# Kernel optimization log

Hardware: AMD Instinct MI355X
Metric: run time of the kernel (lower is better)

## Reference

```python
import jax, jax.numpy as jnp
import numpy as np

NB = 5  # frequency bands


def _ln(x, g, b, eps=1e-5):
    m = jnp.mean(x, axis=-1, keepdims=True)
    v = jnp.var(x, axis=-1, keepdims=True)
    return (x - m) / jnp.sqrt(v + eps) * g + b


def _graph_adj(x, adj_w, sw1, sb1, sw2, sb2, pos_factor, pos_enc):
    # x: [B, D, N] -> degree-normalized adjacency [B, N, N]
    d = x.shape[1]
    xt = jnp.swapaxes(x, 1, 2)  # [B, N, D]
    # concat-MLP first layer split: cat(xi, xj) @ W1 == xi @ W1[:d] + xj @ W1[d:]
    a = xt @ sw1[:d]
    bpart = xt @ sw1[d:]
    h = jax.nn.elu(a[:, :, None, :] + bpart[:, None, :, :] + sb1)  # [B, N, N, H]
    dyn = jax.nn.sigmoid(jnp.squeeze(h @ sw2, -1) + sb2)  # [B, N, N]
    static = jax.nn.softmax(adj_w, axis=-1)
    pos = jax.nn.softmax(pos_enc, axis=-1)
    comb = jax.nn.softmax(static + dyn + pos_factor * pos, axis=-1)
    deg = jnp.sum(comb, axis=-1)
    dis = (deg + 1e-8) ** -0.5
    return dis[:, :, None] * comb * dis[:, None, :]


def _gcn(x, adj, w, b):
    # x: [B, D, N], adj: [B, N, N] -> [B, D_out, N]
    xt = jnp.swapaxes(x, 1, 2)
    out = jnp.einsum('bij,bjd->bid', adj, xt) @ w + b
    return jnp.swapaxes(out, 1, 2)


def _mha(x, qkv_w, qkv_b, ow, ob, nh=4):
    B, S, D = x.shape
    dh = D // nh
    q, k, v = jnp.split(x @ qkv_w + qkv_b, 3, axis=-1)
    q = q.reshape(B, S, nh, dh)
    k = k.reshape(B, S, nh, dh)
    v = v.reshape(B, S, nh, dh)
    att = jax.nn.softmax(jnp.einsum('bihd,bjhd->bhij', q, k) / float(np.sqrt(dh)), axis=-1)
    o = jnp.einsum('bhij,bjhd->bihd', att, v).reshape(B, S, D)
    return o @ ow + ob


def setup_inputs():
    key = jax.random.key(0)
    B, D, N = 16, 256, 64
    ks = iter(jax.random.split(key, 40))

    def rn(shape, s=0.05):
        return jax.random.normal(next(ks), shape, dtype=jnp.float32) * s

    eyeN = jnp.eye(N, dtype=jnp.float32)
    return dict(
        feature=jax.random.normal(next(ks), (B, NB * D, 1, N), dtype=jnp.float32),
        l_adj_w=jnp.tile(eyeN[None], (NB, 1, 1)),
        l_sim_w1=rn((NB, 2 * D, D)), l_sim_b1=jnp.zeros((NB, D), jnp.float32),
        l_sim_w2=rn((NB, D, 1)), l_sim_b2=jnp.zeros((NB, 1), jnp.float32),
        l_pos_factor=jnp.full((NB,), 0.5, jnp.float32),
        l_pos_enc=jnp.tile(eyeN[None], (NB, 1, 1)),
        l_gcn_w=rn((NB, D, D)), l_gcn_b=jnp.zeros((NB, D), jnp.float32),
        g_adj_w=jnp.eye(NB, dtype=jnp.float32),
        g_sim_w1=rn((2 * D, D)), g_sim_b1=jnp.zeros((D,), jnp.float32),
        g_sim_w2=rn((D, 1)), g_sim_b2=jnp.zeros((1,), jnp.float32),
        g_pos_factor=jnp.float32(0.5),
        g_pos_enc=jnp.eye(NB, dtype=jnp.float32),
        g_gcn_w=rn((D, D)), g_gcn_b=jnp.zeros((D,), jnp.float32),
        qkv_w=rn((D, 3 * D)), qkv_b=jnp.zeros((3 * D,), jnp.float32),
        attn_ow=rn((D, D)), attn_ob=jnp.zeros((D,), jnp.float32),
        ln1_g=jnp.ones((D,), jnp.float32), ln1_b=jnp.zeros((D,), jnp.float32),
        ln2_g=jnp.ones((D,), jnp.float32), ln2_b=jnp.zeros((D,), jnp.float32),
        mlp_w1=rn((D, 4 * D)), mlp_b1=jnp.zeros((4 * D,), jnp.float32),
        mlp_w2=rn((4 * D, D)), mlp_b2=jnp.zeros((D,), jnp.float32),
        imp_w=rn((NB, N, 1)), imp_b=jnp.zeros((NB, 1), jnp.float32),
    )


def reference(feature, l_adj_w, l_sim_w1, l_sim_b1, l_sim_w2, l_sim_b2,
              l_pos_factor, l_pos_enc, l_gcn_w, l_gcn_b,
              g_adj_w, g_sim_w1, g_sim_b1, g_sim_w2, g_sim_b2,
              g_pos_factor, g_pos_enc, g_gcn_w, g_gcn_b,
              qkv_w, qkv_b, attn_ow, attn_ob,
              ln1_g, ln1_b, ln2_g, ln2_b,
              mlp_w1, mlp_b1, mlp_w2, mlp_b2,
              imp_w, imp_b):
    B = feature.shape[0]
    D = l_gcn_w.shape[-1]
    N = feature.shape[-1]
    # [B, 5*D, 1, N] -> [5, B, D, N] band-major
    x5 = jnp.moveaxis(feature.reshape(B, NB, D, N), 1, 0)
    # per-band local graphs + GCNs (vmapped over the 5 bands)
    local_adj = jax.vmap(_graph_adj)(x5, l_adj_w, l_sim_w1, l_sim_b1,
                                     l_sim_w2, l_sim_b2, l_pos_factor, l_pos_enc)
    local_out = jax.vmap(_gcn)(x5, local_adj, l_gcn_w, l_gcn_b)  # [5, B, D, N]
    scale_nodes = jnp.moveaxis(jnp.mean(local_out, axis=-1), 0, 1)  # [B, 5, D]
    # cross-band attention block (pre: MHA + residual + LN, then MLP + residual + LN)
    attn = _mha(scale_nodes, qkv_w, qkv_b, attn_ow, attn_ob)
    h1 = _ln(scale_nodes + attn, ln1_g, ln1_b)
    mlp = jax.nn.gelu(h1 @ mlp_w1 + mlp_b1, approximate=False) @ mlp_w2 + mlp_b2
    se = _ln(h1 + mlp, ln2_g, ln2_b)  # [B, 5, D]
    # global scale graph over the 5 band nodes
    xg = jnp.swapaxes(se, 1, 2)  # [B, D, 5]
    g_adj = _graph_adj(xg, g_adj_w, g_sim_w1, g_sim_b1, g_sim_w2, g_sim_b2,
                       g_pos_factor, g_pos_enc)
    g_out = jnp.swapaxes(_gcn(xg, g_adj, g_gcn_w, g_gcn_b), 1, 2)  # [B, 5, D]
    # modulate each local band feature by its global scale vector
    enh = local_out * jnp.moveaxis(g_out, 1, 0)[..., None]  # [5, B, D, N]
    # per-band importance projection over channels: [5, B, D, 1]
    out5 = jnp.einsum('kbdn,kno->kbdo', enh, imp_w) + imp_b[:, None, None, :]
    output = jnp.moveaxis(out5, 0, 1).reshape(B, NB * D, 1, 1)
    return output, g_adj, jnp.moveaxis(local_out, 0, 1)
```

## Files before the change

### kernel.cpp

```cpp
#include <hip/hip_runtime.h>
#include <hip/hip_bf16.h>

#define NBANDS 5
#define BATCH  16
#define DIM    256
#define NNODE  64
#define SEQ    5
#define NHEAD  4
#define DHEAD  64

typedef __hip_bfloat16 bf16;
typedef unsigned short ushort_t;
typedef __attribute__((ext_vector_type(8))) short short8;
typedef __attribute__((ext_vector_type(4))) float float4v;

__device__ __forceinline__ float bu2f(ushort_t u){
    bf16 h = *reinterpret_cast<bf16*>(&u);
    return __bfloat162float(h);
}
__device__ __forceinline__ ushort_t f2bu(float x){
    bf16 h = __float2bfloat16(x);
    return *reinterpret_cast<ushort_t*>(&h);
}

__global__ void k_bases(const float* __restrict__ l_adj_w, const float* __restrict__ l_pos_enc,
                        const float* __restrict__ l_pf,
                        const float* __restrict__ g_adj_w, const float* __restrict__ g_pos_enc,
                        const float* __restrict__ g_pf,
                        float* __restrict__ sbase, float* __restrict__ gbase,
                        float* __restrict__ zbuf)
{
    int blk = blockIdx.x;
    int t = threadIdx.x;
    if (blk < NBANDS*NNODE) {
        int k = blk / NNODE, i = blk % NNODE;
        float aw = l_adj_w[(k*NNODE + i)*NNODE + t];
        float pe = l_pos_enc[(k*NNODE + i)*NNODE + t];
        float m1 = aw, m2 = pe;
        for (int o=32;o>0;o>>=1){ m1 = fmaxf(m1, __shfl_xor(m1,o,64)); m2 = fmaxf(m2, __shfl_xor(m2,o,64)); }
        float e1 = __expf(aw-m1), e2 = __expf(pe-m2);
        float s1=e1, s2=e2;
        for (int o=32;o>0;o>>=1){ s1 += __shfl_xor(s1,o,64); s2 += __shfl_xor(s2,o,64); }
        float pf = l_pf[k];
        sbase[(k*NNODE+i)*NNODE + t] = e1/s1 + pf*(e2/s2);
    } else if (blk == NBANDS*NNODE) {
        if (t < NBANDS) {
            int i = t;
            float r1[NBANDS], r2[NBANDS];
            float m1=-1e30f, m2=-1e30f;
            for (int j=0;j<NBANDS;j++){
                r1[j]=g_adj_w[i*NBANDS+j]; r2[j]=g_pos_enc[i*NBANDS+j];
                m1=fmaxf(m1,r1[j]); m2=fmaxf(m2,r2[j]);
            }
            float s1=0.f,s2=0.f;
            for (int j=0;j<NBANDS;j++){ r1[j]=__expf(r1[j]-m1); r2[j]=__expf(r2[j]-m2); s1+=r1[j]; s2+=r2[j]; }
            float pf = g_pf[0];
            for (int j=0;j<NBANDS;j++) gbase[i*NBANDS+j] = r1[j]/s1 + pf*(r2[j]/s2);
        }
    } else {
        for (int i=t;i<DIM;i+=64) zbuf[i] = 0.f;
    }
}

__global__ void k_prep(const float* __restrict__ w1, const float* __restrict__ gw,
                       ushort_t* __restrict__ w1bt, ushort_t* __restrict__ gwbt)
{
    int blk = blockIdx.x;
    int inst = blk >> 4;
    int t = blk & 15;
    int r0 = (t>>2)*64, c0 = (t&3)*64;
    const float* src; ushort_t* dst;
    if (inst < 10){
        int k = inst>>1, half = inst&1;
        src = w1  + ((size_t)k*512 + half*256)*256;
        dst = w1bt+ ((size_t)k*512 + half*256)*256;
    } else {
        int k = inst-10;
        src = gw  + (size_t)k*65536;
        dst = gwbt+ (size_t)k*65536;
    }
    __shared__ ushort_t tile[64][65];
    int tid = threadIdx.x;
    int jj = tid & 63, i4 = tid >> 6;
    for (int p=0;p<16;p++){
        int i = p*4 + i4;
        tile[i][jj] = f2bu(src[(size_t)(r0+i)*256 + c0 + jj]);
    }
    __syncthreads();
    for (int p=0;p<16;p++){
        int i = p*4 + i4;
        dst[(size_t)(c0+i)*256 + r0 + jj] = tile[jj][i];
    }
}

__global__ void k_transpose_feat(const float* __restrict__ feat,
                                 ushort_t* __restrict__ xtb,
                                 ushort_t* __restrict__ xtT)
{
    int k = blockIdx.x / BATCH, b = blockIdx.x % BATCH;
    __shared__ ushort_t tile[64][65];
    const float* src = feat + ((size_t)b*NBANDS*DIM + (size_t)k*DIM)*NNODE;
    ushort_t* dst = xtb + (size_t)(k*BATCH+b)*NNODE*DIM;
    int tid = threadIdx.x;
    ushort_t* dstT = xtT + (size_t)(k*BATCH+b)*DIM*NNODE;
    for (int u=0; u<64; ++u){
        int idx = u*256 + tid;
        dstT[idx] = f2bu(src[idx]);
    }
    for (int dt=0; dt<4; ++dt){
        for (int r=0;r<16;r++){
            int dp = r*4 + (tid>>6);
            int n  = tid & 63;
            tile[dp][n] = f2bu(src[(size_t)(dt*64+dp)*NNODE + n]);
        }
        __syncthreads();
        for (int r=0;r<16;r++){
            int n  = r*4 + (tid>>6);
            int dp = tid & 63;
            dst[(size_t)n*DIM + dt*64 + dp] = tile[dp][n];
        }
        __syncthreads();
    }
}

__global__ void __launch_bounds__(256) k_ab_mfma(const ushort_t* __restrict__ xtb,
                        const ushort_t* __restrict__ w1bt, const float* __restrict__ b1,
                        ushort_t* __restrict__ aab, ushort_t* __restrict__ bbb)
{
    int blk = blockIdx.x;
    int kband = blk / (BATCH*8);
    int b = (blk/8) % BATCH;
    int nblk = blk & 7;
    int tid = threadIdx.x;
    int wave = tid>>6, lane = tid&63;
    int c16 = lane & 15, quad = lane >> 4;
    int m0 = wave*16;
    size_t rowbase = (size_t)(kband*BATCH+b)*NNODE;
    const ushort_t* Aptr = xtb + (rowbase + m0 + c16)*DIM + quad*8;
    const ushort_t* Bbase = w1bt + (size_t)kband*512*DIM;
    int ncol0 = nblk*64;
    const ushort_t* Bptr0 = Bbase + (size_t)(ncol0 +  0 + c16)*DIM + quad*8;
    const ushort_t* Bptr1 = Bbase + (size_t)(ncol0 + 16 + c16)*DIM + quad*8;
    const ushort_t* Bptr2 = Bbase + (size_t)(ncol0 + 32 + c16)*DIM + quad*8;
    const ushort_t* Bptr3 = Bbase + (size_t)(ncol0 + 48 + c16)*DIM + quad*8;
    float4v acc0 = {0.f,0.f,0.f,0.f}, acc1 = acc0, acc2 = acc0, acc3 = acc0;
    #pragma unroll
    for (int ks=0; ks<8; ++ks){
        short8 a  = *reinterpret_cast<const short8*>(Aptr  + ks*32);
        short8 b0 = *reinterpret_cast<const short8*>(Bptr0 + ks*32);
        short8 b1v= *reinterpret_cast<const short8*>(Bptr1 + ks*32);
        short8 b2 = *reinterpret_cast<const short8*>(Bptr2 + ks*32);
        short8 b3 = *reinterpret_cast<const short8*>(Bptr3 + ks*32);
        acc0 = __builtin_amdgcn_mfma_f32_16x16x32_bf16(a, b0, acc0, 0,0,0);
        acc1 = __builtin_amdgcn_mfma_f32_16x16x32_bf16(a, b1v, acc1, 0,0,0);
        acc2 = __builtin_amdgcn_mfma_f32_16x16x32_bf16(a, b2, acc2, 0,0,0);
        acc3 = __builtin_amdgcn_mfma_f32_16x16x32_bf16(a, b3, acc3, 0,0,0);
    }
    int half = nblk >> 2;
    int cbase = (nblk & 3)*64;
    ushort_t* dst = half ? bbb : aab;
    float4v accs[4] = {acc0, acc1, acc2, acc3};
    #pragma unroll
    for (int nt=0; nt<4; ++nt){
        int cg = cbase + nt*16 + c16;
        float bias = half ? 0.f : b1[kband*DIM + cg];
        #pragma unroll
        for (int r=0;r<4;r++){
            int m = m0 + quad*4 + r;
            dst[(rowbase + m)*DIM + cg] = f2bu(accs[nt][r] + bias);
        }
    }
}

__global__ void k_dyn_comb(const ushort_t* __restrict__ aab,
                           const ushort_t* __restrict__ bbb,
                           const float* __restrict__ w2, const float* __restrict__ b2arr,
                           const float* __restrict__ sbase,
                           ushort_t* __restrict__ combb)
{
    int blk = blockIdx.x;
    int k = blk / (BATCH*16);
    int b = (blk / 16) % BATCH;
    int i0 = (blk % 16) * 4;
    int kb = k*BATCH + b;
    __shared__ float arows[4][DIM];
    __shared__ float w2s[DIM];
    __shared__ float dyn_s[4][NNODE];
    int tid = threadIdx.x;
    int wave = tid >> 6, lane = tid & 63;
    for (int r=0;r<4;r++) arows[r][tid] = bu2f(aab[((size_t)kb*NNODE + i0 + r)*DIM + tid]);
    w2s[tid] = w2[k*DIM + tid];
    __syncthreads();
    const ushort_t* bpbase = bbb + (size_t)kb*NNODE*DIM;
    for (int jt=0; jt<16; ++jt){
        int j = jt*4 + wave;
        const ushort_t* bj = bpbase + (size_t)j*DIM;
        float acc[4] = {0.f,0.f,0.f,0.f};
        #pragma unroll
        for (int m=0;m<4;m++){
            int dd = lane + m*64;
            float bpv = bu2f(bj[dd]);
            float wv  = w2s[dd];
            #pragma unroll
            for (int r=0;r<4;r++){
                float v = arows[r][dd] + bpv;
                float e = (v > 0.f) ? v : (__expf(v) - 1.f);
                acc[r] += e*wv;
            }
        }
        #pragma unroll
        for (int r=0;r<4;r++){
            float s = acc[r];
            for (int o=32;o>0;o>>=1) s += __shfl_xor(s,o,64);
            if (lane==0) dyn_s[r][j] = s;
        }
    }
    __syncthreads();
    {
        float sb2 = b2arr[k];
        float t = dyn_s[wave][lane] + sb2;
        float sg = 1.f/(1.f + __expf(-t));
        float val = sbase[(k*NNODE + i0 + wave)*NNODE + lane] + sg;
        float m = val;
        for (int o=32;o>0;o>>=1) m = fmaxf(m, __shfl_xor(m,o,64));
        float e = __expf(val - m);
        float s = e;
        for (int o=32;o>0;o>>=1) s += __shfl_xor(s,o,64);
        combb[((size_t)kb*NNODE + i0 + wave)*NNODE + lane] = f2bu(e/s);
    }
}

__global__ void __launch_bounds__(256) k_y_mfma(const ushort_t* __restrict__ combb,
                       const ushort_t* __restrict__ xtT,
                       ushort_t* __restrict__ yb)
{
    int blk = blockIdx.x;
    int kband = blk / (BATCH*4);
    int b = (blk/4) % BATCH;
    int nblk = blk & 3;
    int tid = threadIdx.x;
    int wave = tid>>6, lane = tid&63;
    int c16 = lane & 15, quad = lane >> 4;
    int m0 = wave*16;
    int kb = kband*BATCH + b;
    const ushort_t* Aptr = combb + ((size_t)kb*NNODE + m0 + c16)*NNODE + quad*8;
    const ushort_t* Bbase = xtT + (size_t)kb*DIM*NNODE;
    int ncol0 = nblk*64;
    const ushort_t* Bptr0 = Bbase + (size_t)(ncol0 +  0 + c16)*NNODE + quad*8;
    const ushort_t* Bptr1 = Bbase + (size_t)(ncol0 + 16 + c16)*NNODE + quad*8;
    const ushort_t* Bptr2 = Bbase + (size_t)(ncol0 + 32 + c16)*NNODE + quad*8;
    const ushort_t* Bptr3 = Bbase + (size_t)(ncol0 + 48 + c16)*NNODE + quad*8;
    float4v acc0 = {0.f,0.f,0.f,0.f}, acc1 = acc0, acc2 = acc0, acc3 = acc0;
    #pragma unroll
    for (int ks=0; ks<2; ++ks){
        short8 a  = *reinterpret_cast<const short8*>(Aptr  + ks*32);
        short8 b0 = *reinterpret_cast<const short8*>(Bptr0 + ks*32);
        short8 b1v= *reinterpret_cast<const short8*>(Bptr1 + ks*32);
        short8 b2 = *reinterpret_cast<const short8*>(Bptr2 + ks*32);
        short8 b3 = *reinterpret_cast<const short8*>(Bptr3 + ks*32);
        acc0 = __builtin_amdgcn_mfma_f32_16x16x32_bf16(a, b0, acc0, 0,0,0);
        acc1 = __builtin_amdgcn_mfma_f32_16x16x32_bf16(a, b1v, acc1, 0,0,0);
        acc2 = __builtin_amdgcn_mfma_f32_16x16x32_bf16(a, b2, acc2, 0,0,0);
        acc3 = __builtin_amdgcn_mfma_f32_16x16x32_bf16(a, b3, acc3, 0,0,0);
    }
    size_t rowbase = (size_t)kb*NNODE;
    float4v accs[4] = {acc0, acc1, acc2, acc3};
    #pragma unroll
    for (int nt=0; nt<4; ++nt){
        int cg = ncol0 + nt*16 + c16;
        #pragma unroll
        for (int r=0;r<4;r++){
            int m = m0 + quad*4 + r;
            yb[(rowbase + m)*DIM + cg] = f2bu(accs[nt][r]);
        }
    }
}

__global__ void __launch_bounds__(256) k_gcn_mfma(const ushort_t* __restrict__ yb,
                         const ushort_t* __restrict__ gwbt, const float* __restrict__ gb,
                         float* __restrict__ out_local)
{
    int blk = blockIdx.x;
    int kband = blk / (BATCH*4);
    int b = (blk/4) % BATCH;
    int nblk = blk & 3;
    int tid = threadIdx.x;
    int wave = tid>>6, lane = tid&63;
    int c16 = lane & 15, quad = lane >> 4;
    int m0 = wave*16;
    int kb = kband*BATCH + b;
    const ushort_t* Aptr = yb + ((size_t)kb*NNODE + m0 + c16)*DIM + quad*8;
    const ushort_t* Bbase = gwbt + (size_t)kband*DIM*DIM;
    int ncol0 = nblk*64;
    const ushort_t* Bptr0 = Bbase + (size_t)(ncol0 +  0 + c16)*DIM + quad*8;
    const ushort_t* Bptr1 = Bbase + (size_t)(ncol0 + 16 + c16)*DIM + quad*8;
    const ushort_t* Bptr2 = Bbase + (size_t)(ncol0 + 32 + c16)*DIM + quad*8;
    const ushort_t* Bptr3 = Bbase + (size_t)(ncol0 + 48 + c16)*DIM + quad*8;
    float4v acc0 = {0.f,0.f,0.f,0.f}, acc1 = acc0, acc2 = acc0, acc3 = acc0;
    #pragma unroll
    for (int ks=0; ks<8; ++ks){
        short8 a  = *reinterpret_cast<const short8*>(Aptr  + ks*32);
        short8 b0 = *reinterpret_cast<const short8*>(Bptr0 + ks*32);
        short8 b1v= *reinterpret_cast<const short8*>(Bptr1 + ks*32);
        short8 b2 = *reinterpret_cast<const short8*>(Bptr2 + ks*32);
        short8 b3 = *reinterpret_cast<const short8*>(Bptr3 + ks*32);
        acc0 = __builtin_amdgcn_mfma_f32_16x16x32_bf16(a, b0, acc0, 0,0,0);
        acc1 = __builtin_amdgcn_mfma_f32_16x16x32_bf16(a, b1v, acc1, 0,0,0);
        acc2 = __builtin_amdgcn_mfma_f32_16x16x32_bf16(a, b2, acc2, 0,0,0);
        acc3 = __builtin_amdgcn_mfma_f32_16x16x32_bf16(a, b3, acc3, 0,0,0);
    }
    float4v accs[4] = {acc0, acc1, acc2, acc3};
    #pragma unroll
    for (int nt=0; nt<4; ++nt){
        int cg = ncol0 + nt*16 + c16;
        float bias = gb[kband*DIM + cg];
        float4 v = make_float4(accs[nt][0]+bias, accs[nt][1]+bias, accs[nt][2]+bias, accs[nt][3]+bias);
        float* dst = out_local + ((size_t)(b*NBANDS + kband)*DIM + cg)*NNODE + m0 + quad*4;
        *reinterpret_cast<float4*>(dst) = v;
    }
}

__global__ void k_scale(const float* __restrict__ out_local, float* __restrict__ scalew)
{
    int k = blockIdx.x / BATCH, b = blockIdx.x % BATCH;
    int d = threadIdx.x;
    const float4* zl = reinterpret_cast<const float4*>(out_local + ((size_t)(b*NBANDS + k)*DIM + d)*NNODE);
    float acc = 0.f;
    #pragma unroll
    for (int q=0;q<16;++q){
        float4 v = zl[q];
        acc += v.x + v.y + v.z + v.w;
    }
    scalew[((size_t)b*SEQ + k)*DIM + d] = acc * (1.f/64.f);
}

template<int COLS, int SLICES>
__global__ void __launch_bounds__(256) k_gemv(const float* __restrict__ x, const float* __restrict__ w,
                       const float* __restrict__ bias, float* __restrict__ out,
                       int K, int N, int act)
{
    int chunks = N / COLS;
    int row = blockIdx.x / chunks;
    int n0 = (blockIdx.x % chunks) * COLS;
    int c = threadIdx.x % COLS, s = threadIdx.x / COLS;
    __shared__ float xs[1024];
    __shared__ float part[SLICES][COLS];
    for (int i = threadIdx.x; i < K; i += 256) xs[i] = x[(size_t)row*K + i];
    __syncthreads();
    int klen = K / SLICES;
    const float* wp = w + (size_t)(s*klen)*N + n0 + c;
    const float* xp = xs + s*klen;
    float acc = 0.f;
    #pragma unroll 8
    for (int i = 0; i < klen; ++i) acc += xp[i] * wp[(size_t)i*N];
    part[s][c] = acc;
    __syncthreads();
    if (s == 0){
        float v = bias[n0+c];
        #pragma unroll
        for (int q=0;q<SLICES;q++) v += part[q][c];
        if (act) v = 0.5f*v*(1.f + erff(v*0.70710678118654752f));
        out[(size_t)row*N + n0 + c] = v;
    }
}

__global__ void k_attn(const float* __restrict__ qkvw, float* __restrict__ ows)
{
    int b = blockIdx.x;
    int tid = threadIdx.x;
    int h = tid >> 6, l = tid & 63;
    __shared__ float att[NHEAD][SEQ][SEQ];
    const float* base = qkvw + (size_t)b*SEQ*3*DIM;
    for (int i=0;i<SEQ;i++){
        float qv = base[(size_t)i*3*DIM + h*DHEAD + l];
        for (int j=0;j<SEQ;j++){
            float kv = base[(size_t)j*3*DIM + DIM + h*DHEAD + l];
            float p = qv * kv;
            for (int o=32;o>0;o>>=1) p += __shfl_xor(p,o,64);
            if (l==0) att[h][i][j] = p * 0.125f;
        }
    }
    __syncthreads();
    if (l == 0){
        for (int i=0;i<SEQ;i++){
            float m=-1e30f;
            for (int j=0;j<SEQ;j++) m = fmaxf(m, att[h][i][j]);
            float e[SEQ]; float s=0.f;
            for (int j=0;j<SEQ;j++){ e[j] = __expf(att[h][i][j]-m); s+=e[j]; }
            for (int j=0;j<SEQ;j++) att[h][i][j] = e[j]/s;
        }
    }
    __syncthreads();
    for (int i=0;i<SEQ;i++){
        float acc=0.f;
        for (int j=0;j<SEQ;j++) acc += att[h][i][j] * base[(size_t)j*3*DIM + 2*DIM + h*DHEAD + l];
        ows[((size_t)b*SEQ + i)*DIM + h*DHEAD + l] = acc;
    }
}

__device__ __forceinline__ float block_ln(float v, int tid, float* red, float g, float bln)
{
    float s = v;
    for (int o=32;o>0;o>>=1) s += __shfl_xor(s,o,64);
    int wave = tid>>6, lane = tid&63;
    if (lane==0) red[wave] = s;
    __syncthreads();
    float mean = (red[0]+red[1]+red[2]+red[3]) * (1.f/DIM);
    float c = v - mean;
    float q = c*c;
    for (int o=32;o>0;o>>=1) q += __shfl_xor(q,o,64);
    __syncthreads();
    if (lane==0) red[wave] = q;
    __syncthreads();
    float var = (red[0]+red[1]+red[2]+red[3]) * (1.f/DIM);
    return c * rsqrtf(var + 1e-5f) * g + bln;
}

__global__ void k_ln(const float* __restrict__ a, const float* __restrict__ r,
                     const float* __restrict__ g, const float* __restrict__ be,
                     float* __restrict__ out)
{
    int row = blockIdx.x;
    int d = threadIdx.x;
    __shared__ float red[4];
    float v = a[(size_t)row*DIM + d] + r[(size_t)row*DIM + d];
    out[(size_t)row*DIM + d] = block_ln(v, d, red, g[d], be[d]);
}

__global__ void k_gadj(const float* __restrict__ gaw, const float* __restrict__ gbw,
                       const float* __restrict__ gw2, const float* __restrict__ gb2,
                       const float* __restrict__ gbase,
                       float* __restrict__ gcombw, float* __restrict__ out_gadj)
{
    int b = blockIdx.x;
    int tid = threadIdx.x;
    int wave = tid>>6, lane = tid&63;
    __shared__ float dyn[SEQ][SEQ];
    __shared__ float w2s[DIM];
    w2s[tid] = gw2[tid];
    __syncthreads();
    for (int p = wave; p < SEQ*SEQ; p += 4){
        int i = p / SEQ, j = p % SEQ;
        const float* gar = gaw + ((size_t)b*SEQ+i)*DIM;
        const float* gbr = gbw + ((size_t)b*SEQ+j)*DIM;
        float acc = 0.f;
        #pragma unroll
        for (int m=0;m<4;m++){
            int dd = lane + m*64;
            float v = gar[dd] + gbr[dd];
            float e = (v>0.f) ? v : (__expf(v)-1.f);
            acc += e * w2s[dd];
        }
        for (int o=32;o>0;o>>=1) acc += __shfl_xor(acc,o,64);
        if (lane==0) dyn[i][j] = acc;
    }
    __syncthreads();
    if (tid < SEQ){
        int i = tid;
        float sb2 = gb2[0];
        float row[SEQ]; float m=-1e30f;
        for (int j=0;j<SEQ;j++){
            float sg = 1.f/(1.f+__expf(-(dyn[i][j]+sb2)));
            row[j] = gbase[i*SEQ+j] + sg;
            m = fmaxf(m,row[j]);
        }
        float ssum=0.f;
        for (int j=0;j<SEQ;j++){ row[j]=__expf(row[j]-m); ssum+=row[j]; }
        for (int j=0;j<SEQ;j++){
            float c = row[j]/ssum;
            gcombw[((size_t)b*SEQ+i)*SEQ + j] = c;
            out_gadj[((size_t)b*SEQ+i)*SEQ + j] = c;
        }
    }
}

__global__ void k_gmix(const float* __restrict__ gcombw, const float* __restrict__ sew,
                       float* __restrict__ trow)
{
    int row = blockIdx.x;
    int b = row / SEQ;
    int d = threadIdx.x;
    float t = 0.f;
    #pragma unroll
    for (int j=0;j<SEQ;j++) t += gcombw[row*SEQ + j] * sew[((size_t)b*SEQ + j)*DIM + d];
    trow[(size_t)row*DIM + d] = t;
}

__global__ void k_final(const float* __restrict__ out_local,
                        const float* __restrict__ goutw,
                        const float* __restrict__ imp_w, const float* __restrict__ imp_b,
                        float* __restrict__ out0)
{
    int b = blockIdx.x / NBANDS, k = blockIdx.x % NBANDS;
    __shared__ float iw[NNODE];
    int d = threadIdx.x;
    if (d < NNODE) iw[d] = imp_w[k*NNODE + d];
    __syncthreads();
    const float4* zl = reinterpret_cast<const float4*>(out_local + ((size_t)(b*NBANDS + k)*DIM + d)*NNODE);
    float acc = 0.f;
    #pragma unroll
    for (int q=0;q<16;++q){
        float4 v = zl[q];
        acc += v.x*iw[q*4] + v.y*iw[q*4+1] + v.z*iw[q*4+2] + v.w*iw[q*4+3];
    }
    float val = goutw[((size_t)b*NBANDS+k)*DIM + d] * acc + imp_b[k];
    out0[((size_t)b*NBANDS+k)*DIM + d] = val;
}

extern "C" void kernel_launch(void* const* d_in, const int* in_sizes, int n_in,
                              void* d_out, int out_size, void* d_ws, size_t ws_size,
                              hipStream_t stream)
{
    const float* feature      = (const float*)d_in[0];
    const float* l_adj_w      = (const float*)d_in[1];
    const float* l_sim_w1     = (const float*)d_in[2];
    const float* l_sim_b1     = (const float*)d_in[3];
    const float* l_sim_w2     = (const float*)d_in[4];
    const float* l_sim_b2     = (const float*)d_in[5];
    const float* l_pos_factor = (const float*)d_in[6];
    const float* l_pos_enc    = (const float*)d_in[7];
    const float* l_gcn_w      = (const float*)d_in[8];
    const float* l_gcn_b      = (const float*)d_in[9];
    const float* g_adj_w      = (const float*)d_in[10];
    const float* g_sim_w1     = (const float*)d_in[11];
    const float* g_sim_b1     = (const float*)d_in[12];
    const float* g_sim_w2     = (const float*)d_in[13];
    const float* g_sim_b2     = (const float*)d_in[14];
    const float* g_pos_factor = (const float*)d_in[15];
    const float* g_pos_enc    = (const float*)d_in[16];
    const float* g_gcn_w      = (const float*)d_in[17];
    const float* g_gcn_b      = (const float*)d_in[18];
    const float* qkv_w        = (const float*)d_in[19];
    const float* qkv_b        = (const float*)d_in[20];
    const float* attn_ow      = (const float*)d_in[21];
    const float* attn_ob      = (const float*)d_in[22];
    const float* ln1_g        = (const float*)d_in[23];
    const float* ln1_b        = (const float*)d_in[24];
    const float* ln2_g        = (const float*)d_in[25];
    const float* ln2_b        = (const float*)d_in[26];
    const float* mlp_w1       = (const float*)d_in[27];
    const float* mlp_b1       = (const float*)d_in[28];
    const float* mlp_w2       = (const float*)d_in[29];
    const float* mlp_b2       = (const float*)d_in[30];
    const float* imp_w        = (const float*)d_in[31];
    const float* imp_b        = (const float*)d_in[32];

    float* out0      = (float*)d_out;
    float* out_gadj  = out0 + (size_t)BATCH*NBANDS*DIM;
    float* out_local = out_gadj + (size_t)BATCH*NBANDS*NBANDS;

    const size_t BIG = (size_t)NBANDS*BATCH*NNODE*DIM;
    ushort_t* xtb   = (ushort_t*)d_ws;
    ushort_t* aab   = xtb + BIG;
    ushort_t* bbb   = aab + BIG;
    ushort_t* xtT   = bbb + BIG;
    ushort_t* yb    = aab;
    ushort_t* w1bt  = xtT + BIG;
    ushort_t* gwbt  = w1bt + (size_t)NBANDS*512*DIM;
    ushort_t* combb = gwbt + (size_t)NBANDS*DIM*DIM;
    float* fp = (float*)(combb + (size_t)NBANDS*BATCH*NNODE*NNODE);
    float* sbase  = fp; fp += NBANDS*NNODE*NNODE;
    float* gbase  = fp; fp += 32;
    float* zbuf   = fp; fp += DIM;
    float* scalew = fp; fp += BATCH*SEQ*DIM;
    float* qkvw   = fp; fp += BATCH*SEQ*3*DIM;
    float* ows    = fp; fp += BATCH*SEQ*DIM;
    float* projw  = fp; fp += BATCH*SEQ*DIM;
    float* h1w    = fp; fp += BATCH*SEQ*DIM;
    float* mhw    = fp; fp += BATCH*SEQ*4*DIM;
    float* m2w    = fp; fp += BATCH*SEQ*DIM;
    float* sew    = fp; fp += BATCH*SEQ*DIM;
    float* gaw    = fp; fp += BATCH*SEQ*DIM;
    float* gbw    = fp; fp += BATCH*SEQ*DIM;
    float* gcombw = fp; fp += 512;
    float* trow   = fp; fp += BATCH*SEQ*DIM;
    float* goutw  = fp; fp += BATCH*SEQ*DIM;

    const int ROWS = BATCH*SEQ;

    k_bases<<<NBANDS*NNODE + 2, 64, 0, stream>>>(l_adj_w, l_pos_enc, l_pos_factor,
                                                 g_adj_w, g_pos_enc, g_pos_factor,
                                                 sbase, gbase, zbuf);
    k_prep<<<240, 256, 0, stream>>>(l_sim_w1, l_gcn_w, w1bt, gwbt);
    k_transpose_feat<<<NBANDS*BATCH, 256, 0, stream>>>(feature, xtb, xtT);
    k_ab_mfma<<<NBANDS*BATCH*8, 256, 0, stream>>>(xtb, w1bt, l_sim_b1, aab, bbb);
    k_dyn_comb<<<NBANDS*BATCH*16, 256, 0, stream>>>(aab, bbb, l_sim_w2, l_sim_b2, sbase, combb);
    k_y_mfma<<<NBANDS*BATCH*4, 256, 0, stream>>>(combb, xtT, yb);
    k_gcn_mfma<<<NBANDS*BATCH*4, 256, 0, stream>>>(yb, gwbt, l_gcn_b, out_local);
    k_scale<<<NBANDS*BATCH, 256, 0, stream>>>(out_local, scalew);
    k_gemv<64,4><<<ROWS*12, 256, 0, stream>>>(scalew, qkv_w, qkv_b, qkvw, 256, 768, 0);
    k_attn<<<BATCH, 256, 0, stream>>>(qkvw, ows);
    k_gemv<64,4><<<ROWS*4, 256, 0, stream>>>(ows, attn_ow, attn_ob, projw, 256, 256, 0);
    k_ln<<<ROWS, 256, 0, stream>>>(projw, scalew, ln1_g, ln1_b, h1w);
    k_gemv<64,4><<<ROWS*16, 256, 0, stream>>>(h1w, mlp_w1, mlp_b1, mhw, 256, 1024, 1);
    k_gemv<32,8><<<ROWS*8, 256, 0, stream>>>(mhw, mlp_w2, mlp_b2, m2w, 1024, 256, 0);
    k_ln<<<ROWS, 256, 0, stream>>>(m2w, h1w, ln2_g, ln2_b, sew);
    k_gemv<64,4><<<ROWS*4, 256, 0, stream>>>(sew, g_sim_w1, g_sim_b1, gaw, 256, 256, 0);
    k_gemv<64,4><<<ROWS*4, 256, 0, stream>>>(sew, g_sim_w1 + (size_t)DIM*DIM, zbuf, gbw, 256, 256, 0);
    k_gadj<<<BATCH, 256, 0, stream>>>(gaw, gbw, g_sim_w2, g_sim_b2, gbase, gcombw, out_gadj);
    k_gmix<<<ROWS, 256, 0, stream>>>(gcombw, sew, trow);
    k_gemv<64,4><<<ROWS*4, 256, 0, stream>>>(trow, g_gcn_w, g_gcn_b, goutw, 256, 256, 0);
    k_final<<<BATCH*NBANDS, 256, 0, stream>>>(out_local, goutw, imp_w, imp_b, out0);
}
```

Baseline: 264.7 us.

## Fuse setup kernels, LN into GEMVs, and restructure dyn_comb with LDS staging

Merges the three setup kernels into one launch and fuses each LayerNorm into the following GEMV (MLP1, and both halves of the global sim projection). The gmix step is folded into the global GCN GEMV, and the importance-weighted reduction moves into the scale kernel so the final kernel becomes elementwise. k_dyn_comb now stages the whole B-part tile in LDS and gives each thread one (i,j) pair, which removes the per-j wave shuffle reductions. Together these cut launch count and intermediate global traffic, at the cost of recomputing LayerNorm in every column block and using more LDS per block in dyn_comb.

```diff
diff --git a/kernel.cpp b/kernel.cpp
--- a/kernel.cpp
+++ b/kernel.cpp
@@ -23,17 +23,25 @@
     return *reinterpret_cast<ushort_t*>(&h);
 }
 
-__global__ void k_bases(const float* __restrict__ l_adj_w, const float* __restrict__ l_pos_enc,
-                        const float* __restrict__ l_pf,
-                        const float* __restrict__ g_adj_w, const float* __restrict__ g_pos_enc,
-                        const float* __restrict__ g_pf,
-                        float* __restrict__ sbase, float* __restrict__ gbase,
-                        float* __restrict__ zbuf)
+__global__ void __launch_bounds__(256) k_head(
+    const float* __restrict__ l_adj_w, const float* __restrict__ l_pos_enc,
+    const float* __restrict__ l_pf,
+    const float* __restrict__ g_adj_w, const float* __restrict__ g_pos_enc,
+    const float* __restrict__ g_pf,
+    float* __restrict__ sbase, float* __restrict__ gbase,
+    const float* __restrict__ w1, const float* __restrict__ gw,
+    ushort_t* __restrict__ w1bt, ushort_t* __restrict__ gwbt,
+    const float* __restrict__ feat,
+    ushort_t* __restrict__ xtb, ushort_t* __restrict__ xtT)
 {
     int blk = blockIdx.x;
-    int t = threadIdx.x;
-    if (blk < NBANDS*NNODE) {
-        int k = blk / NNODE, i = blk % NNODE;
+    int tid = threadIdx.x;
+    __shared__ ushort_t tile[64][65];
+
+    if (blk < 80) {
+        int r = blk*4 + (tid>>6);
+        int k = r >> 6, i = r & 63;
+        int t = tid & 63;
         float aw = l_adj_w[(k*NNODE + i)*NNODE + t];
         float pe = l_pos_enc[(k*NNODE + i)*NNODE + t];
         float m1 = aw, m2 = pe;
@@ -43,9 +51,9 @@
         for (int o=32;o>0;o>>=1){ s1 += __shfl_xor(s1,o,64); s2 += __shfl_xor(s2,o,64); }
         float pf = l_pf[k];
         sbase[(k*NNODE+i)*NNODE + t] = e1/s1 + pf*(e2/s2);
-    } else if (blk == NBANDS*NNODE) {
-        if (t < NBANDS) {
-            int i = t;
+    } else if (blk == 80) {
+        if (tid < NBANDS) {
+            int i = tid;
             float r1[NBANDS], r2[NBANDS];
             float m1=-1e30f, m2=-1e30f;
             for (int j=0;j<NBANDS;j++){
@@ -57,69 +65,55 @@
             float pf = g_pf[0];
             for (int j=0;j<NBANDS;j++) gbase[i*NBANDS+j] = r1[j]/s1 + pf*(r2[j]/s2);
         }
+    } else if (blk < 321) {
+        int idx = blk - 81;
+        int inst = idx >> 4;
+        int t = idx & 15;
+        int r0 = (t>>2)*64, c0 = (t&3)*64;
+        const float* src; ushort_t* dst;
+        if (inst < 10){
+            int k = inst>>1, half = inst&1;
+            src = w1  + ((size_t)k*512 + half*256)*256;
+            dst = w1bt+ ((size_t)k*512 + half*256)*256;
+        } else {
+            int k = inst-10;
+            src = gw  + (size_t)k*65536;
+            dst = gwbt+ (size_t)k*65536;
+        }
+        int jj = tid & 63, i4 = tid >> 6;
+        for (int p=0;p<16;p++){
+            int i = p*4 + i4;
+            tile[i][jj] = f2bu(src[(size_t)(r0+i)*256 + c0 + jj]);
+        }
+        __syncthreads();
+        for (int p=0;p<16;p++){
+            int i = p*4 + i4;
+            dst[(size_t)(c0+i)*256 + r0 + jj] = tile[jj][i];
+        }
     } else {
-        for (int i=t;i<DIM;i+=64) zbuf[i] = 0.f;
-    }
-}
-
-__global__ void k_prep(const float* __restrict__ w1, const float* __restrict__ gw,
-                       ushort_t* __restrict__ w1bt, ushort_t* __restrict__ gwbt)
-{
-    int blk = blockIdx.x;
-    int inst = blk >> 4;
-    int t = blk & 15;
-    int r0 = (t>>2)*64, c0 = (t&3)*64;
-    const float* src; ushort_t* dst;
-    if (inst < 10){
-        int k = inst>>1, half = inst&1;
-        src = w1  + ((size_t)k*512 + half*256)*256;
-        dst = w1bt+ ((size_t)k*512 + half*256)*256;
-    } else {
-        int k = inst-10;
-        src = gw  + (size_t)k*65536;
-        dst = gwbt+ (size_t)k*65536;
-    }
-    __shared__ ushort_t tile[64][65];
-    int tid = threadIdx.x;
-    int jj = tid & 63, i4 = tid >> 6;
-    for (int p=0;p<16;p++){
-        int i = p*4 + i4;
-        tile[i][jj] = f2bu(src[(size_t)(r0+i)*256 + c0 + jj]);
-    }
-    __syncthreads();
-    for (int p=0;p<16;p++){
-        int i = p*4 + i4;
-        dst[(size_t)(c0+i)*256 + r0 + jj] = tile[jj][i];
-    }
-}
-
-__global__ void k_transpose_feat(const float* __restrict__ feat,
-                                 ushort_t* __restrict__ xtb,
-                                 ushort_t* __restrict__ xtT)
-{
-    int k = blockIdx.x / BATCH, b = blockIdx.x % BATCH;
-    __shared__ ushort_t tile[64][65];
-    const float* src = feat + ((size_t)b*NBANDS*DIM + (size_t)k*DIM)*NNODE;
-    ushort_t* dst = xtb + (size_t)(k*BATCH+b)*NNODE*DIM;
-    int tid = threadIdx.x;
-    ushort_t* dstT = xtT + (size_t)(k*BATCH+b)*DIM*NNODE;
-    for (int u=0; u<64; ++u){
-        int idx = u*256 + tid;
-        dstT[idx] = f2bu(src[idx]);
-    }
-    for (int dt=0; dt<4; ++dt){
-        for (int r=0;r<16;r++){
-            int dp = r*4 + (tid>>6);
-            int n  = tid & 63;
-            tile[dp][n] = f2bu(src[(size_t)(dt*64+dp)*NNODE + n]);
-        }
-        __syncthreads();
-        for (int r=0;r<16;r++){
-            int n  = r*4 + (tid>>6);
-            int dp = tid & 63;
-            dst[(size_t)n*DIM + dt*64 + dp] = tile[dp][n];
-        }
-        __syncthreads();
+        int idx = blk - 321;
+        int k = idx / BATCH, b = idx % BATCH;
+        const float* src = feat + ((size_t)b*NBANDS*DIM + (size_t)k*DIM)*NNODE;
+        ushort_t* dst = xtb + (size_t)(k*BATCH+b)*NNODE*DIM;
+        ushort_t* dstT = xtT + (size_t)(k*BATCH+b)*DIM*NNODE;
+        for (int u=0; u<64; ++u){
+            int i = u*256 + tid;
+            dstT[i] = f2bu(src[i]);
+        }
+        for (int dt=0; dt<4; ++dt){
+            for (int r=0;r<16;r++){
+                int dp = r*4 + (tid>>6);
+                int n  = tid & 63;
+                tile[dp][n] = f2bu(src[(size_t)(dt*64+dp)*NNODE + n]);
+            }
+            __syncthreads();
+            for (int r=0;r<16;r++){
+                int n  = r*4 + (tid>>6);
+                int dp = tid & 63;
+                dst[(size_t)n*DIM + dt*64 + dp] = tile[dp][n];
+            }
+            __syncthreads();
+        }
     }
 }
 
@@ -172,7 +166,7 @@
     }
 }
 
-__global__ void k_dyn_comb(const ushort_t* __restrict__ aab,
+__global__ void __launch_bounds__(256) k_dyn_comb(const ushort_t* __restrict__ aab,
                            const ushort_t* __restrict__ bbb,
                            const float* __restrict__ w2, const float* __restrict__ b2arr,
                            const float* __restrict__ sbase,
@@ -183,51 +177,48 @@
     int b = (blk / 16) % BATCH;
     int i0 = (blk % 16) * 4;
     int kb = k*BATCH + b;
+    __shared__ ushort_t bs[64][260];
     __shared__ float arows[4][DIM];
     __shared__ float w2s[DIM];
-    __shared__ float dyn_s[4][NNODE];
     int tid = threadIdx.x;
     int wave = tid >> 6, lane = tid & 63;
+    const ushort_t* bsrc = bbb + (size_t)kb*NNODE*DIM;
+    for (int u=0; u<16; ++u){
+        int idx = u*1024 + tid*4;
+        int row = idx >> 8, col = idx & 255;
+        *reinterpret_cast<ushort4*>(&bs[row][col]) =
+            *reinterpret_cast<const ushort4*>(&bsrc[(size_t)row*DIM + col]);
+    }
     for (int r=0;r<4;r++) arows[r][tid] = bu2f(aab[((size_t)kb*NNODE + i0 + r)*DIM + tid]);
     w2s[tid] = w2[k*DIM + tid];
     __syncthreads();
-    const ushort_t* bpbase = bbb + (size_t)kb*NNODE*DIM;
-    for (int jt=0; jt<16; ++jt){
-        int j = jt*4 + wave;
-        const ushort_t* bj = bpbase + (size_t)j*DIM;
-        float acc[4] = {0.f,0.f,0.f,0.f};
-        #pragma unroll
-        for (int m=0;m<4;m++){
-            int dd = lane + m*64;
-            float bpv = bu2f(bj[dd]);
-            float wv  = w2s[dd];
-            #pragma unroll
-            for (int r=0;r<4;r++){
-                float v = arows[r][dd] + bpv;
-                float e = (v > 0.f) ? v : (__expf(v) - 1.f);
-                acc[r] += e*wv;
-            }
-        }
-        #pragma unroll
-        for (int r=0;r<4;r++){
-            float s = acc[r];
-            for (int o=32;o>0;o>>=1) s += __shfl_xor(s,o,64);
-            if (lane==0) dyn_s[r][j] = s;
-        }
-    }
-    __syncthreads();
-    {
-        float sb2 = b2arr[k];
-        float t = dyn_s[wave][lane] + sb2;
-        float sg = 1.f/(1.f + __expf(-t));
-        float val = sbase[(k*NNODE + i0 + wave)*NNODE + lane] + sg;
-        float m = val;
-        for (int o=32;o>0;o>>=1) m = fmaxf(m, __shfl_xor(m,o,64));
-        float e = __expf(val - m);
-        float s = e;
-        for (int o=32;o>0;o>>=1) s += __shfl_xor(s,o,64);
-        combb[((size_t)kb*NNODE + i0 + wave)*NNODE + lane] = f2bu(e/s);
-    }
+
+    int i = i0 + wave;
+    float acc = 0.f;
+    #pragma unroll 4
+    for (int dd=0; dd<64; ++dd){
+        ushort4 bv = *reinterpret_cast<const ushort4*>(&bs[lane][dd*4]);
+        float4 av = *reinterpret_cast<const float4*>(&arows[wave][dd*4]);
+        float4 wv = *reinterpret_cast<const float4*>(&w2s[dd*4]);
+        float v0 = av.x + bu2f(bv.x);
+        float v1 = av.y + bu2f(bv.y);
+        float v2 = av.z + bu2f(bv.z);
+        float v3 = av.w + bu2f(bv.w);
+        float e0 = (v0>0.f)? v0 : (__expf(v0)-1.f);
+        float e1 = (v1>0.f)? v1 : (__expf(v1)-1.f);
+        float e2 = (v2>0.f)? v2 : (__expf(v2)-1.f);
+        float e3 = (v3>0.f)? v3 : (__expf(v3)-1.f);
+        acc += e0*wv.x + e1*wv.y + e2*wv.z + e3*wv.w;
+    }
+    float sb2 = b2arr[k];
+    float sg = 1.f/(1.f + __expf(-(acc + sb2)));
+    float val = sbase[(k*NNODE + i)*NNODE + lane] + sg;
+    float m = val;
+    for (int o=32;o>0;o>>=1) m = fmaxf(m, __shfl_xor(m,o,64));
+    float e = __expf(val - m);
+    float s = e;
+    for (int o=32;o>0;o>>=1) s += __shfl_xor(s,o,64);
+    combb[((size_t)kb*NNODE + i)*NNODE + lane] = f2bu(e/s);
 }
 
 __global__ void __launch_bounds__(256) k_y_mfma(const ushort_t* __restrict__ combb,
@@ -320,18 +311,24 @@
     }
 }
 
-__global__ void k_scale(const float* __restrict__ out_local, float* __restrict__ scalew)
+__global__ void k_scale2(const float* __restrict__ out_local, const float* __restrict__ imp_w,
+                         float* __restrict__ scalew, float* __restrict__ impw)
 {
     int k = blockIdx.x / BATCH, b = blockIdx.x % BATCH;
     int d = threadIdx.x;
+    __shared__ float iw[NNODE];
+    if (d < NNODE) iw[d] = imp_w[k*NNODE + d];
+    __syncthreads();
     const float4* zl = reinterpret_cast<const float4*>(out_local + ((size_t)(b*NBANDS + k)*DIM + d)*NNODE);
-    float acc = 0.f;
+    float s = 0.f, di = 0.f;
     #pragma unroll
     for (int q=0;q<16;++q){
         float4 v = zl[q];
-        acc += v.x + v.y + v.z + v.w;
-    }
-    scalew[((size_t)b*SEQ + k)*DIM + d] = acc * (1.f/64.f);
+        s  += v.x + v.y + v.z + v.w;
+        di += v.x*iw[q*4] + v.y*iw[q*4+1] + v.z*iw[q*4+2] + v.w*iw[q*4+3];
+    }
+    scalew[((size_t)b*SEQ + k)*DIM + d] = s * (1.f/64.f);
+    impw[((size_t)b*SEQ + k)*DIM + d]   = di;
 }
 
 template<int COLS, int SLICES>
@@ -416,15 +413,74 @@
     return c * rsqrtf(var + 1e-5f) * g + bln;
 }
 
-__global__ void k_ln(const float* __restrict__ a, const float* __restrict__ r,
-                     const float* __restrict__ g, const float* __restrict__ be,
-                     float* __restrict__ out)
-{
-    int row = blockIdx.x;
-    int d = threadIdx.x;
+__global__ void __launch_bounds__(256) k_mlp1_ln(const float* __restrict__ projw,
+                         const float* __restrict__ scalew,
+                         const float* __restrict__ ln1_g, const float* __restrict__ ln1_b,
+                         const float* __restrict__ w1, const float* __restrict__ b1,
+                         float* __restrict__ h1w, float* __restrict__ mhw)
+{
+    int row = blockIdx.x / 16;
+    int n0 = (blockIdx.x % 16) * 64;
+    int tid = threadIdx.x;
+    __shared__ float xs[DIM];
     __shared__ float red[4];
-    float v = a[(size_t)row*DIM + d] + r[(size_t)row*DIM + d];
-    out[(size_t)row*DIM + d] = block_ln(v, d, red, g[d], be[d]);
+    __shared__ float part[4][64];
+    float v = projw[(size_t)row*DIM + tid] + scalew[(size_t)row*DIM + tid];
+    float h = block_ln(v, tid, red, ln1_g[tid], ln1_b[tid]);
+    xs[tid] = h;
+    if ((blockIdx.x % 16) == 0) h1w[(size_t)row*DIM + tid] = h;
+    __syncthreads();
+    int c = tid & 63, s = tid >> 6;
+    const float* wp = w1 + (size_t)(s*64)*1024 + n0 + c;
+    const float* xp = xs + s*64;
+    float acc = 0.f;
+    #pragma unroll 8
+    for (int i=0;i<64;++i) acc += xp[i] * wp[(size_t)i*1024];
+    part[s][c] = acc;
+    __syncthreads();
+    if (s == 0){
+        float o = b1[n0+c] + part[0][c] + part[1][c] + part[2][c] + part[3][c];
+        o = 0.5f*o*(1.f + erff(o*0.70710678118654752f));
+        mhw[(size_t)row*1024 + n0 + c] = o;
+    }
+}
+
+__global__ void __launch_bounds__(256) k_gab_ln(const float* __restrict__ m2w,
+                        const float* __restrict__ h1w,
+                        const float* __restrict__ ln2_g, const float* __restrict__ ln2_b,
+                        const float* __restrict__ gw1, const float* __restrict__ gb1,
+                        float* __restrict__ sew, float* __restrict__ gaw, float* __restrict__ gbw)
+{
+    int row = blockIdx.x / 4;
+    int n0 = (blockIdx.x % 4) * 64;
+    int tid = threadIdx.x;
+    __shared__ float xs[DIM];
+    __shared__ float red[4];
+    __shared__ float partA[4][64];
+    __shared__ float partB[4][64];
+    float v = m2w[(size_t)row*DIM + tid] + h1w[(size_t)row*DIM + tid];
+    float h = block_ln(v, tid, red, ln2_g[tid], ln2_b[tid]);
+    xs[tid] = h;
+    if ((blockIdx.x % 4) == 0) sew[(size_t)row*DIM + tid] = h;
+    __syncthreads();
+    int c = tid & 63, s = tid >> 6;
+    const float* wpA = gw1 + (size_t)(s*64)*DIM + n0 + c;
+    const float* wpB = wpA + (size_t)DIM*DIM;
+    const float* xp = xs + s*64;
+    float aA = 0.f, aB = 0.f;
+    #pragma unroll 8
+    for (int i=0;i<64;++i){
+        float xv = xp[i];
+        aA += xv * wpA[(size_t)i*DIM];
+        aB += xv * wpB[(size_t)i*DIM];
+    }
+    partA[s][c] = aA;
+    partB[s][c] = aB;
+    __syncthreads();
+    if (s == 0){
+        gaw[(size_t)row*DIM + n0 + c] = gb1[n0+c] + partA[0][c]+partA[1][c]+partA[2][c]+partA[3][c];
+        gbw[(size_t)row*DIM + n0 + c] = partB[0][c]+partB[1][c]+partB[2][c]+partB[3][c];
+    }
 }
 
 __global__ void k_gadj(const float* __restrict__ gaw, const float* __restrict__ gbw,
@@ -474,37 +530,42 @@
     }
 }
 
-__global__ void k_gmix(const float* __restrict__ gcombw, const float* __restrict__ sew,
-                       float* __restrict__ trow)
+__global__ void __launch_bounds__(256) k_gout_mix(const float* __restrict__ gcombw,
+                         const float* __restrict__ sew,
+                         const float* __restrict__ ggw, const float* __restrict__ ggb,
+                         float* __restrict__ goutw)
+{
+    int row = blockIdx.x / 4;
+    int n0 = (blockIdx.x % 4) * 64;
+    int b = row / SEQ;
+    int tid = threadIdx.x;
+    __shared__ float xs[DIM];
+    __shared__ float part[4][64];
+    float t = 0.f;
+    #pragma unroll
+    for (int j=0;j<SEQ;j++) t += gcombw[row*SEQ + j] * sew[((size_t)b*SEQ + j)*DIM + tid];
+    xs[tid] = t;
+    __syncthreads();
+    int c = tid & 63, s = tid >> 6;
+    const float* wp = ggw + (size_t)(s*64)*DIM + n0 + c;
+    const float* xp = xs + s*64;
+    float acc = 0.f;
+    #pragma unroll 8
+    for (int i=0;i<64;++i) acc += xp[i] * wp[(size_t)i*DIM];
+    part[s][c] = acc;
+    __syncthreads();
+    if (s == 0){
+        goutw[(size_t)row*DIM + n0 + c] = ggb[n0+c] + part[0][c]+part[1][c]+part[2][c]+part[3][c];
+    }
+}
+
+__global__ void k_final(const float* __restrict__ impw, const float* __restrict__ goutw,
+                        const float* __restrict__ imp_b, float* __restrict__ out0)
 {
     int row = blockIdx.x;
-    int b = row / SEQ;
+    int k = row % NBANDS;
     int d = threadIdx.x;
-    float t = 0.f;
-    #pragma unroll
-    for (int j=0;j<SEQ;j++) t += gcombw[row*SEQ + j] * sew[((size_t)b*SEQ + j)*DIM + d];
-    trow[(size_t)row*DIM + d] = t;
-}
-
-__global__ void k_final(const float* __restrict__ out_local,
-                        const float* __restrict__ goutw,
-                        const float* __restrict__ imp_w, const float* __restrict__ imp_b,
-                        float* __restrict__ out0)
-{
-    int b = blockIdx.x / NBANDS, k = blockIdx.x % NBANDS;
-    __shared__ float iw[NNODE];
-    int d = threadIdx.x;
-    if (d < NNODE) iw[d] = imp_w[k*NNODE + d];
-    __syncthreads();
-    const float4* zl = reinterpret_cast<const float4*>(out_local + ((size_t)(b*NBANDS + k)*DIM + d)*NNODE);
-    float acc = 0.f;
-    #pragma unroll
-    for (int q=0;q<16;++q){
-        float4 v = zl[q];
-        acc += v.x*iw[q*4] + v.y*iw[q*4+1] + v.z*iw[q*4+2] + v.w*iw[q*4+3];
-    }
-    float val = goutw[((size_t)b*NBANDS+k)*DIM + d] * acc + imp_b[k];
-    out0[((size_t)b*NBANDS+k)*DIM + d] = val;
+    out0[(size_t)row*DIM + d] = goutw[(size_t)row*DIM + d] * impw[(size_t)row*DIM + d] + imp_b[k];
 }
 
 extern "C" void kernel_launch(void* const* d_in, const int* in_sizes, int n_in,
@@ -561,8 +622,8 @@
     float* fp = (float*)(combb + (size_t)NBANDS*BATCH*NNODE*NNODE);
     float* sbase  = fp; fp += NBANDS*NNODE*NNODE;
     float* gbase  = fp; fp += 32;
-    float* zbuf   = fp; fp += DIM;
     float* scalew = fp; fp += BATCH*SEQ*DIM;
+    float* impw   = fp; fp += BATCH*SEQ*DIM;
     float* qkvw   = fp; fp += BATCH*SEQ*3*DIM;
     float* ows    = fp; fp += BATCH*SEQ*DIM;
     float* projw  = fp; fp += BATCH*SEQ*DIM;
@@ -573,32 +634,27 @@
     float* gaw    = fp; fp += BATCH*SEQ*DIM;
     float* gbw    = fp; fp += BATCH*SEQ*DIM;
     float* gcombw = fp; fp += 512;
-    float* trow   = fp; fp += BATCH*SEQ*DIM;
     float* goutw  = fp; fp += BATCH*SEQ*DIM;
 
     const int ROWS = BATCH*SEQ;
 
-    k_bases<<<NBANDS*NNODE + 2, 64, 0, stream>>>(l_adj_w, l_pos_enc, l_pos_factor,
-                                                 g_adj_w, g_pos_enc, g_pos_factor,
-                                                 sbase, gbase, zbuf);
-    k_prep<<<240, 256, 0, stream>>>(l_sim_w1, l_gcn_w, w1bt, gwbt);
-    k_transpose_feat<<<NBANDS*BATCH, 256, 0, stream>>>(feature, xtb, xtT);
+    k_head<<<401, 256, 0, stream>>>(l_adj_w, l_pos_enc, l_pos_factor,
+                                    g_adj_w, g_pos_enc, g_pos_factor,
+                                    sbase, gbase,
+                                    l_sim_w1, l_gcn_w, w1bt, gwbt,
+                                    feature, xtb, xtT);
     k_ab_mfma<<<NBANDS*BATCH*8, 256, 0, stream>>>(xtb, w1bt, l_sim_b1, aab, bbb);
     k_dyn_comb<<<NBANDS*BATCH*16, 256, 0, stream>>>(aab, bbb, l_sim_w2, l_sim_b2, sbase, combb);
     k_y_mfma<<<NBANDS*BATCH*4, 256, 0, stream>>>(combb, xtT, yb);
     k_gcn_mfma<<<NBANDS*BATCH*4, 256, 0, stream>>>(yb, gwbt, l_gcn_b, out_local);
-    k_scale<<<NBANDS*BATCH, 256, 0, stream>>>(out_local, scalew);
+    k_scale2<<<NBANDS*BATCH, 256, 0, stream>>>(out_local, imp_w, scalew, impw);
     k_gemv<64,4><<<ROWS*12, 256, 0, stream>>>(scalew, qkv_w, qkv_b, qkvw, 256, 768, 0);
     k_attn<<<BATCH, 256, 0, stream>>>(qkvw, ows);
     k_gemv<64,4><<<ROWS*4, 256, 0, stream>>>(ows, attn_ow, attn_ob, projw, 256, 256, 0);
-    k_ln<<<ROWS, 256, 0, stream>>>(projw, scalew, ln1_g, ln1_b, h1w);
-    k_gemv<64,4><<<ROWS*16, 256, 0, stream>>>(h1w, mlp_w1, mlp_b1, mhw, 256, 1024, 1);
+    k_mlp1_ln<<<ROWS*16, 256, 0, stream>>>(projw, scalew, ln1_g, ln1_b, mlp_w1, mlp_b1, h1w, mhw);
     k_gemv<32,8><<<ROWS*8, 256, 0, stream>>>(mhw, mlp_w2, mlp_b2, m2w, 1024, 256, 0);
-    k_ln<<<ROWS, 256, 0, stream>>>(m2w, h1w, ln2_g, ln2_b, sew);
-    k_gemv<64,4><<<ROWS*4, 256, 0, stream>>>(sew, g_sim_w1, g_sim_b1, gaw, 256, 256, 0);
-    k_gemv<64,4><<<ROWS*4, 256, 0, stream>>>(sew, g_sim_w1 + (size_t)DIM*DIM, zbuf, gbw, 256, 256, 0);
+    k_gab_ln<<<ROWS*4, 256, 0, stream>>>(m2w, h1w, ln2_g, ln2_b, g_sim_w1, g_sim_b1, sew, gaw, gbw);
     k_gadj<<<BATCH, 256, 0, stream>>>(gaw, gbw, g_sim_w2, g_sim_b2, gbase, gcombw, out_gadj);
-    k_gmix<<<ROWS, 256, 0, stream>>>(gcombw, sew, trow);
-    k_gemv<64,4><<<ROWS*4, 256, 0, stream>>>(trow, g_gcn_w, g_gcn_b, goutw, 256, 256, 0);
-    k_final<<<BATCH*NBANDS, 256, 0, stream>>>(out_local, goutw, imp_w, imp_b, out0);
-}
+    k_gout_mix<<<ROWS*4, 256, 0, stream>>>(gcombw, sew, g_gcn_w, g_gcn_b, goutw);
+    k_final<<<ROWS, 256, 0, stream>>>(impw, goutw, imp_b, out0);
+}
```

Result: faster. 240.3 us (-9.2%).
